# Kernel tuning notes

Hardware: AMD Instinct MI355X
Metric: run time of the kernel (lower is better)

The kernel has to match this reference:

```python
import jax, jax.numpy as jnp
import numpy as np

NU, NI, NA = 100000, 50000, 5000
FEAT, H, L = 256, 128, 2
E_RATES, E_SIM, E_HAS = 1000000, 500000, 250000
SCALE = 0.05


def setup_inputs() -> dict:
    key = jax.random.key(0)
    ks = jax.random.split(key, 20)
    f32 = jnp.float32
    inp = {}
    inp["x_item_feat"] = jax.random.normal(ks[0], (NI, FEAT), f32)
    inp["user_emb"] = jax.random.normal(ks[1], (NU, H), f32) * SCALE
    inp["attr_emb"] = jax.random.normal(ks[2], (NA, H), f32) * SCALE
    inp["lin_item_W"] = jax.random.normal(ks[3], (FEAT, H), f32) * SCALE
    inp["lin_item_b"] = jnp.zeros((H,), f32)
    inp["ui_Wl"] = jax.random.normal(ks[4], (L, 4, H, H), f32) * SCALE
    inp["ui_bl"] = jnp.zeros((L, 4, H), f32)
    inp["ui_Wr"] = jax.random.normal(ks[5], (L, 4, H, H), f32) * SCALE
    inp["ii_Wl"] = jax.random.normal(ks[6], (L, 2, H, H), f32) * SCALE
    inp["ii_bl"] = jnp.zeros((L, 2, H), f32)
    inp["ii_Wr"] = jax.random.normal(ks[7], (L, 2, H, H), f32) * SCALE
    inp["ia_Wl"] = jax.random.normal(ks[8], (L, 4, H, H), f32) * SCALE
    inp["ia_bl"] = jnp.zeros((L, 4, H), f32)
    inp["ia_Wr"] = jax.random.normal(ks[9], (L, 4, H, H), f32) * SCALE
    inp["alpha"] = jnp.zeros((3,), f32)
    # edge_index rows: [src; dst], ranges per node type
    inp["edge_rates"] = jnp.stack([
        jax.random.randint(ks[10], (E_RATES,), 0, NU, jnp.int32),   # user src
        jax.random.randint(ks[11], (E_RATES,), 0, NI, jnp.int32)])  # item dst
    inp["edge_sim"] = jnp.stack([
        jax.random.randint(ks[12], (E_SIM,), 0, NI, jnp.int32),
        jax.random.randint(ks[13], (E_SIM,), 0, NI, jnp.int32)])
    inp["edge_has"] = jnp.stack([
        jax.random.randint(ks[14], (E_HAS,), 0, NI, jnp.int32),    # item src
        jax.random.randint(ks[15], (E_HAS,), 0, NA, jnp.int32)])   # attr dst
    return inp


def _sage_edge(x_src, x_dst, src, dst, Wl, bl, Wr):
    # PyG SAGEConv: lin_l(mean of neighbor messages) + lin_r(root)
    n_dst = x_dst.shape[0]
    agg = jax.ops.segment_sum(x_src[src], dst, num_segments=n_dst)
    cnt = jax.ops.segment_sum(jnp.ones(src.shape[0], x_src.dtype), dst, num_segments=n_dst)
    agg = agg / jnp.maximum(cnt, 1.0)[:, None]
    return agg @ Wl + bl + x_dst @ Wr


def _sage_self(x, Wl, bl, Wr):
    # 'self' relation realized as identity self-loops: mean aggr of single self neighbor = x
    return x @ Wl + bl + x @ Wr


def reference(x_item_feat, user_emb, attr_emb, lin_item_W, lin_item_b,
              ui_Wl, ui_bl, ui_Wr, ii_Wl, ii_bl, ii_Wr, ia_Wl, ia_bl, ia_Wr,
              alpha, edge_rates, edge_sim, edge_has):
    x_item = x_item_feat @ lin_item_W + lin_item_b
    relu = jax.nn.relu

    # user-item branch (relations: 0=rates u->i, 1=rev_rates i->u, 2=user self, 3=item self)
    hu, hi = user_emb, x_item
    for l in range(L):
        o_i = 0.5 * (_sage_edge(hu, hi, edge_rates[0], edge_rates[1], ui_Wl[l, 0], ui_bl[l, 0], ui_Wr[l, 0])
                     + _sage_self(hi, ui_Wl[l, 3], ui_bl[l, 3], ui_Wr[l, 3]))
        o_u = 0.5 * (_sage_edge(hi, hu, edge_rates[1], edge_rates[0], ui_Wl[l, 1], ui_bl[l, 1], ui_Wr[l, 1])
                     + _sage_self(hu, ui_Wl[l, 2], ui_bl[l, 2], ui_Wr[l, 2]))
        hu, hi = relu(o_u), relu(o_i)
    h_ui_item = hi

    # item-item content branch (0=sim, 1=item self)
    h = x_item
    for l in range(L):
        o = 0.5 * (_sage_edge(h, h, edge_sim[0], edge_sim[1], ii_Wl[l, 0], ii_bl[l, 0], ii_Wr[l, 0])
                   + _sage_self(h, ii_Wl[l, 1], ii_bl[l, 1], ii_Wr[l, 1]))
        h = relu(o)
    h_ii_item = h

    # item-attr branch (0=has i->a, 1=rev_has a->i, 2=item self, 3=attr self)
    hi2, ha = x_item, attr_emb
    for l in range(L):
        o_a = 0.5 * (_sage_edge(hi2, ha, edge_has[0], edge_has[1], ia_Wl[l, 0], ia_bl[l, 0], ia_Wr[l, 0])
                     + _sage_self(ha, ia_Wl[l, 3], ia_bl[l, 3], ia_Wr[l, 3]))
        o_i = 0.5 * (_sage_edge(ha, hi2, edge_has[1], edge_has[0], ia_Wl[l, 1], ia_bl[l, 1], ia_Wr[l, 1])
                     + _sage_self(hi2, ia_Wl[l, 2], ia_bl[l, 2], ia_Wr[l, 2]))
        hi2, ha = relu(o_i), relu(o_a)
    h_ia_item = hi2

    w = jax.nn.softmax(alpha)
    h_fused = w[0] * h_ui_item + w[1] * h_ii_item + w[2] * h_ia_item
    return (h_fused, h_ui_item, h_ii_item, h_ia_item, w)
```

## Files before the change

kernel.cpp:

```cpp
#include <hip/hip_runtime.h>

#define NU_ 100000
#define NI_ 50000
#define NA_ 5000
#define FEAT_ 256
#define H_ 128
#define ER_ 1000000
#define ES_ 500000
#define EH_ 250000

#define NTOT_ (3 * NI_ + NU_ + NA_)
#define RTOT_ (2 * ER_ + ES_ + 2 * EH_)
#define NSB_ ((NTOT_ + 1023) / 1024)
#define B_RI 0
#define B_RU (NI_)
#define B_SI (NI_ + NU_)
#define B_HA (2 * NI_ + NU_)
#define B_HI (2 * NI_ + NU_ + NA_)

typedef long long i64;
typedef unsigned short u16;
typedef unsigned int u32;
typedef __attribute__((ext_vector_type(8))) short bf16x8;
typedef __attribute__((ext_vector_type(4))) float f32x4;

__device__ __forceinline__ u16 f2bf(float v) {
    u32 b = __float_as_uint(v);
    b += 0x7fff + ((b >> 16) & 1);
    return (u16)(b >> 16);
}
__device__ __forceinline__ float bf2f(u16 v) {
    return __uint_as_float((u32)v << 16);
}

__global__ __launch_bounds__(256) void tobf2_kernel(const float4* __restrict__ inU,
                                                    ushort4* __restrict__ outU, long n4u,
                                                    const float4* __restrict__ inA,
                                                    ushort4* __restrict__ outA, long n4a) {
    long i = (long)blockIdx.x * 256 + threadIdx.x;
    const float4* in; ushort4* out;
    if (i < n4u) { in = inU + i; out = outU + i; }
    else if (i < n4u + n4a) { in = inA + (i - n4u); out = outA + (i - n4u); }
    else return;
    float4 v = *in;
    ushort4 o;
    o.x = f2bf(v.x); o.y = f2bf(v.y); o.z = f2bf(v.z); o.w = f2bf(v.w);
    *out = o;
}

__device__ __forceinline__ void rec_of(int r, const int* __restrict__ er,
                                       const int* __restrict__ es,
                                       const int* __restrict__ eh,
                                       int& node, int& val) {
    if (r < 2 * ER_) {
        int e = r >> 1;
        if ((r & 1) == 0) { node = B_RI + er[ER_ + e]; val = er[e]; }
        else              { node = B_RU + er[e];       val = er[ER_ + e]; }
    } else if (r < 2 * ER_ + ES_) {
        int e = r - 2 * ER_;
        node = B_SI + es[ES_ + e]; val = es[e];
    } else {
        int q = r - 2 * ER_ - ES_;
        int e = q >> 1;
        if ((q & 1) == 0) { node = B_HA + eh[EH_ + e]; val = eh[e]; }
        else              { node = B_HI + eh[e];       val = eh[EH_ + e]; }
    }
}

__global__ __launch_bounds__(256) void sbinit_kernel(int* __restrict__ sbc,
                                                     int* __restrict__ OFF) {
    int t = threadIdx.x;
    sbc[t] = t << 16;
    if (t < 4) OFF[t] = 0;
}

__global__ __launch_bounds__(256) void binA_kernel(const int* __restrict__ er,
                                                   const int* __restrict__ es,
                                                   const int* __restrict__ eh,
                                                   int* __restrict__ sbc,
                                                   int* __restrict__ cpool) {
    __shared__ int h[256];
    __shared__ int gof[256];
    int t = threadIdx.x;
    h[t] = 0;
    __syncthreads();
    int base = blockIdx.x * 4096;
    int sbs[16];
    u32 recs[16];
#pragma unroll
    for (int i = 0; i < 16; ++i) {
        int r = base + i * 256 + t;
        sbs[i] = -1;
        if (r < RTOT_) {
            int node, val;
            rec_of(r, er, es, eh, node, val);
            int sb = node >> 10;
            sbs[i] = sb;
            recs[i] = ((u32)(node & 1023) << 17) | (u32)val;
            atomicAdd(&h[sb], 1);
        }
    }
    __syncthreads();
    {
        int c = h[t];
        if (c > 0) gof[t] = atomicAdd(&sbc[t], c);
        h[t] = 0;
    }
    __syncthreads();
#pragma unroll
    for (int i = 0; i < 16; ++i) {
        if (sbs[i] >= 0) {
            int slot = atomicAdd(&h[sbs[i]], 1);
            cpool[gof[sbs[i]] + slot] = (int)recs[i];
        }
    }
}

__global__ __launch_bounds__(256) void sbscan_kernel(const int* __restrict__ sbc,
                                                     int* __restrict__ sbb) {
    int t = threadIdx.x;
    int v = (t < NSB_) ? (sbc[t] - (t << 16)) : 0;
    int incl = v;
    int lane = t & 63;
#pragma unroll
    for (int d = 1; d < 64; d <<= 1) {
        int u = __shfl_up(incl, d);
        if (lane >= d) incl += u;
    }
    __shared__ int wsum[4];
    if (lane == 63) wsum[t >> 6] = incl;
    __syncthreads();
    int wo = 0;
    for (int i = 0; i < (t >> 6); ++i) wo += wsum[i];
    if (t < NSB_) sbb[t] = wo + incl - v;
}

__global__ __launch_bounds__(1024) void binB_kernel(const int* __restrict__ cpool,
                                                    const int* __restrict__ sbb,
                                                    const int* __restrict__ sbc,
                                                    int* __restrict__ off1,
                                                    int* __restrict__ pool) {
    __shared__ int c[1024];
    __shared__ int b[1024];
    __shared__ int wsum[16];
    int sb = blockIdx.x, t = threadIdx.x;
    int rlo = sb << 16, rhi = sbc[sb];
    int base = sbb[sb];
    c[t] = 0;
    __syncthreads();
    for (int j = rlo + t; j < rhi; j += 1024)
        atomicAdd(&c[((u32)cpool[j]) >> 17], 1);
    __syncthreads();
    int v = c[t];
    int incl = v;
    int lane = t & 63;
#pragma unroll
    for (int d = 1; d < 64; d <<= 1) {
        int u = __shfl_up(incl, d);
        if (lane >= d) incl += u;
    }
    if (lane == 63) wsum[t >> 6] = incl;
    __syncthreads();
    int wo = 0;
    for (int i = 0; i < (t >> 6); ++i) wo += wsum[i];
    int ex = wo + incl - v;
    int node = sb * 1024 + t;
    if (node < NTOT_) off1[node] = base + ex + v;
    b[t] = base + ex;
    __syncthreads();
    for (int j = rlo + t; j < rhi; j += 1024) {
        u32 rec = (u32)cpool[j];
        int pos = atomicAdd(&b[rec >> 17], 1);
        pool[pos] = (int)(rec & 0x1FFFF);
    }
}

struct WJob {
    const float* s0; const float* s1; const float* s2;
    int logK; int base;
};
struct WJobs { WJob j[17]; };

__global__ __launch_bounds__(256) void wsplit_kernel(WJobs jobs, int njobs, int total,
                                                     u16* __restrict__ WTH,
                                                     u16* __restrict__ WTL) {
    int gid = blockIdx.x * 256 + threadIdx.x;
    if (gid >= total) return;
    int ji = 0;
    for (int i = 1; i < 17; ++i)
        if (i < njobs && gid >= jobs.j[i].base) ji = i;
    WJob jb = jobs.j[ji];
    int local = gid - jb.base;
    int e = local & 7;
    int l = (local >> 3) & 63;
    int nt = (local >> 9) & 7;
    int kc = local >> 12;
    int n = nt * 16 + (l & 15);
    int k = kc * 32 + ((l >> 4) << 3) + e;
    i64 si = (i64)k * 128 + n;
    float v = jb.s0[si];
    if (jb.s1 != nullptr) v += jb.s1[si] + jb.s2[si];
    if (jb.logK == 8) {
        u32 b = __float_as_uint(v);
        u16 h = (u16)(b >> 16);
        float rem = v - __uint_as_float(b & 0xffff0000u);
        WTH[gid] = h;
        WTL[gid] = (u16)(__float_as_uint(rem) >> 16);
    } else {
        WTH[gid] = f2bf(v);
    }
}

#define ACC8(A, V)                                                            \
    {                                                                         \
        A[0] += bf2f((u16)(V.x & 0xffff)); A[1] += bf2f((u16)(V.x >> 16));    \
        A[2] += bf2f((u16)(V.y & 0xffff)); A[3] += bf2f((u16)(V.y >> 16));    \
        A[4] += bf2f((u16)(V.z & 0xffff)); A[5] += bf2f((u16)(V.z >> 16));    \
        A[6] += bf2f((u16)(V.w & 0xffff)); A[7] += bf2f((u16)(V.w >> 16));    \
    }

struct GOp {
    const u16* feat; const int* off1c; u16* agg;
    int nblk; int n; int pad0; int pad1; int pad2;
};
struct GOps { GOp op[5]; };

__global__ __launch_bounds__(256) void packed_gather_kernel(GOps ops, int nops,
                                                            const int* __restrict__ pool) {
    int b = blockIdx.x;
    int i = 0;
    while (i < nops - 1 && b >= ops.op[i].nblk) { b -= ops.op[i].nblk; ++i; }
    GOp o = ops.op[i];
    int row = b * 16 + (threadIdx.x >> 4);
    if (row >= o.n) return;
    int lane = (threadIdx.x & 15) * 8;
    int start = o.off1c[row - 1];
    int end = o.off1c[row];
    const u16* feat = o.feat;
    float a0[8], a1[8], a2[8], a3[8];
#pragma unroll
    for (int k = 0; k < 8; ++k) { a0[k] = 0.f; a1[k] = 0.f; a2[k] = 0.f; a3[k] = 0.f; }
    int j = start;
    for (; j + 4 <= end; j += 4) {
        int s0 = pool[j], s1 = pool[j + 1], s2 = pool[j + 2], s3 = pool[j + 3];
        uint4 v0 = *(const uint4*)&feat[(i64)s0 * H_ + lane];
        uint4 v1 = *(const uint4*)&feat[(i64)s1 * H_ + lane];
        uint4 v2 = *(const uint4*)&feat[(i64)s2 * H_ + lane];
        uint4 v3 = *(const uint4*)&feat[(i64)s3 * H_ + lane];
        ACC8(a0, v0); ACC8(a1, v1); ACC8(a2, v2); ACC8(a3, v3);
    }
    for (; j < end; ++j) {
        int s0 = pool[j];
        uint4 v0 = *(const uint4*)&feat[(i64)s0 * H_ + lane];
        ACC8(a0, v0);
    }
    float inv = 1.0f / fmaxf((float)(end - start), 1.0f);
    uint4 o4;
    float r0, r1;
    r0 = (a0[0] + a1[0] + a2[0] + a3[0]) * inv; r1 = (a0[1] + a1[1] + a2[1] + a3[1]) * inv;
    o4.x = (u32)f2bf(r0) | ((u32)f2bf(r1) << 16);
    r0 = (a0[2] + a1[2] + a2[2] + a3[2]) * inv; r1 = (a0[3] + a1[3] + a2[3] + a3[3]) * inv;
    o4.y = (u32)f2bf(r0) | ((u32)f2bf(r1) << 16);
    r0 = (a0[4] + a1[4] + a2[4] + a3[4]) * inv; r1 = (a0[5] + a1[5] + a2[5] + a3[5]) * inv;
    o4.z = (u32)f2bf(r0) | ((u32)f2bf(r1) << 16);
    r0 = (a0[6] + a1[6] + a2[6] + a3[6]) * inv; r1 = (a0[7] + a1[7] + a2[7] + a3[7]) * inv;
    o4.w = (u32)f2bf(r0) | ((u32)f2bf(r1) << 16);
    *(uint4*)&o.agg[(i64)row * H_ + lane] = o4;
}

__device__ __forceinline__ void split8(const float* f, bf16x8& h, bf16x8& lo) {
#pragma unroll
    for (int i = 0; i < 8; ++i) {
        u32 b = __float_as_uint(f[i]);
        h[i] = (short)(u16)(b >> 16);
        float rem = f[i] - __uint_as_float(b & 0xffff0000u);
        lo[i] = (short)(u16)(__float_as_uint(rem) >> 16);
    }
}

__global__ __launch_bounds__(256) void mgemm_x_kernel(
    const float* __restrict__ A, const u16* __restrict__ Wh, const u16* __restrict__ Wl,
    const float* __restrict__ bias, u16* __restrict__ Cbf, int M) {
    int t = threadIdx.x;
    int w = t >> 6, l = t & 63;
    int lr = l & 15, lq = l >> 4;
    int m0 = blockIdx.x * 128 + w * 32;

    f32x4 acc[2][8];
#pragma unroll
    for (int mt = 0; mt < 2; ++mt)
#pragma unroll
        for (int nt = 0; nt < 8; ++nt) acc[mt][nt] = (f32x4){0.f, 0.f, 0.f, 0.f};

    for (int kc = 0; kc < 8; ++kc) {
        bf16x8 ah0, al0, ah1, al1;
        {
            int row = m0 + lr;
            float f[8];
            if (row < M) {
                const float* ap = &A[(i64)row * FEAT_ + kc * 32 + lq * 8];
                *(float4*)&f[0] = *(const float4*)ap;
                *(float4*)&f[4] = *(const float4*)(ap + 4);
            } else {
#pragma unroll
                for (int i = 0; i < 8; ++i) f[i] = 0.f;
            }
            split8(f, ah0, al0);
        }
        {
            int row = m0 + 16 + lr;
            float f[8];
            if (row < M) {
                const float* ap = &A[(i64)row * FEAT_ + kc * 32 + lq * 8];
                *(float4*)&f[0] = *(const float4*)ap;
                *(float4*)&f[4] = *(const float4*)(ap + 4);
            } else {
#pragma unroll
                for (int i = 0; i < 8; ++i) f[i] = 0.f;
            }
            split8(f, ah1, al1);
        }
        const u16* whp = Wh + ((i64)kc * 8) * 512 + (i64)l * 8;
        const u16* wlp = Wl + ((i64)kc * 8) * 512 + (i64)l * 8;
#pragma unroll
        for (int nt = 0; nt < 8; ++nt) {
            bf16x8 bh = *(const bf16x8*)(whp + nt * 512);
            bf16x8 bl = *(const bf16x8*)(wlp + nt * 512);
            acc[0][nt] = __builtin_amdgcn_mfma_f32_16x16x32_bf16(ah0, bh, acc[0][nt], 0, 0, 0);
            acc[1][nt] = __builtin_amdgcn_mfma_f32_16x16x32_bf16(ah1, bh, acc[1][nt], 0, 0, 0);
            acc[0][nt] = __builtin_amdgcn_mfma_f32_16x16x32_bf16(al0, bh, acc[0][nt], 0, 0, 0);
            acc[1][nt] = __builtin_amdgcn_mfma_f32_16x16x32_bf16(al1, bh, acc[1][nt], 0, 0, 0);
            acc[0][nt] = __builtin_amdgcn_mfma_f32_16x16x32_bf16(ah0, bl, acc[0][nt], 0, 0, 0);
            acc[1][nt] = __builtin_amdgcn_mfma_f32_16x16x32_bf16(ah1, bl, acc[1][nt], 0, 0, 0);
        }
    }
#pragma unroll
    for (int nt = 0; nt < 8; ++nt) {
        int col = nt * 16 + lr;
        float bb = bias[col];
#pragma unroll
        for (int mt = 0; mt < 2; ++mt) {
#pragma unroll
            for (int r = 0; r < 4; ++r) {
                int row = m0 + mt * 16 + (lq << 2) + r;
                if (row < M) Cbf[(i64)row * H_ + col] = f2bf(acc[mt][nt][r] + bb);
            }
        }
    }
}

struct MOp {
    const u16* A1; const u16* W1; const u16* A2; const u16* W2;
    const float* b1; const float* b2;
    float* C; u16* Cbf;
    int nblk; int n; int fuse; int pad;
};
struct MOps { MOp op[5]; };

__global__ __launch_bounds__(256) void packed_gemm_kernel(
    MOps ops, int nops,
    const float* __restrict__ alpha, const float* __restrict__ fu,
    const float* __restrict__ fi, float* __restrict__ fout,
    float* __restrict__ wout) {
    int blk = blockIdx.x;
    int i = 0;
    while (i < nops - 1 && blk >= ops.op[i].nblk) { blk -= ops.op[i].nblk; ++i; }
    MOp o = ops.op[i];
    int t = threadIdx.x;
    int w = t >> 6, l = t & 63;
    int lr = l & 15, lq = l >> 4;
    int m0 = blk * 128 + w * 32;
    int M = o.n;

    f32x4 acc[2][8];
#pragma unroll
    for (int mt = 0; mt < 2; ++mt)
#pragma unroll
        for (int nt = 0; nt < 8; ++nt) acc[mt][nt] = (f32x4){0.f, 0.f, 0.f, 0.f};

#pragma unroll
    for (int mat = 0; mat < 2; ++mat) {
        const u16* A = mat ? o.A2 : o.A1;
        const u16* W = mat ? o.W2 : o.W1;
#pragma unroll
        for (int kc = 0; kc < 4; ++kc) {
            bf16x8 a0 = {0, 0, 0, 0, 0, 0, 0, 0}, a1 = {0, 0, 0, 0, 0, 0, 0, 0};
            int row0 = m0 + lr, row1 = m0 + 16 + lr;
            if (row0 < M) a0 = *(const bf16x8*)&A[(i64)row0 * H_ + kc * 32 + lq * 8];
            if (row1 < M) a1 = *(const bf16x8*)&A[(i64)row1 * H_ + kc * 32 + lq * 8];
            const u16* wp = W + ((i64)kc * 8) * 512 + (i64)l * 8;
#pragma unroll
            for (int nt = 0; nt < 8; ++nt) {
                bf16x8 bw = *(const bf16x8*)(wp + nt * 512);
                acc[0][nt] = __builtin_amdgcn_mfma_f32_16x16x32_bf16(a0, bw, acc[0][nt], 0, 0, 0);
                acc[1][nt] = __builtin_amdgcn_mfma_f32_16x16x32_bf16(a1, bw, acc[1][nt], 0, 0, 0);
            }
        }
    }

    float w0 = 0.f, w1 = 0.f, w2 = 0.f;
    if (o.fuse) {
        float x0 = alpha[0], x1 = alpha[1], x2 = alpha[2];
        float mx = fmaxf(x0, fmaxf(x1, x2));
        float e0 = __expf(x0 - mx), e1 = __expf(x1 - mx), e2 = __expf(x2 - mx);
        float inv = 1.f / (e0 + e1 + e2);
        w0 = e0 * inv; w1 = e1 * inv; w2 = e2 * inv;
        if (blk == 0 && t == 0) { wout[0] = w0; wout[1] = w1; wout[2] = w2; }
    }

#pragma unroll
    for (int nt = 0; nt < 8; ++nt) {
        int col = nt * 16 + lr;
        float bb = 0.5f * (o.b1[col] + o.b2[col]);
#pragma unroll
        for (int mt = 0; mt < 2; ++mt) {
#pragma unroll
            for (int r = 0; r < 4; ++r) {
                int row = m0 + mt * 16 + (lq << 2) + r;
                if (row < M) {
                    i64 idx = (i64)row * H_ + col;
                    float v = fmaxf(0.5f * acc[mt][nt][r] + bb, 0.f);
                    if (o.C != nullptr) o.C[idx] = v;
                    if (o.Cbf != nullptr) o.Cbf[idx] = f2bf(v);
                    if (o.fuse) fout[idx] = w0 * fu[idx] + w1 * fi[idx] + w2 * v;
                }
            }
        }
    }
}

extern "C" void kernel_launch(void* const* d_in, const int* in_sizes, int n_in,
                              void* d_out, int out_size, void* d_ws, size_t ws_size,
                              hipStream_t stream) {
    const float* xif  = (const float*)d_in[0];
    const float* uemb = (const float*)d_in[1];
    const float* aemb = (const float*)d_in[2];
    const float* liW  = (const float*)d_in[3];
    const float* lib  = (const float*)d_in[4];
    const float* uiWl = (const float*)d_in[5];
    const float* uibl = (const float*)d_in[6];
    const float* uiWr = (const float*)d_in[7];
    const float* iiWl = (const float*)d_in[8];
    const float* iibl = (const float*)d_in[9];
    const float* iiWr = (const float*)d_in[10];
    const float* iaWl = (const float*)d_in[11];
    const float* iabl = (const float*)d_in[12];
    const float* iaWr = (const float*)d_in[13];
    const float* alpha = (const float*)d_in[14];
    const int* er = (const int*)d_in[15];
    const int* es = (const int*)d_in[16];
    const int* eh = (const int*)d_in[17];

    float* out = (float*)d_out;
    float* FUSED  = out;
    float* OUT_UI = out + (i64)NI_ * H_;
    float* OUT_II = out + (i64)2 * NI_ * H_;
    float* OUT_IA = out + (i64)3 * NI_ * H_;
    float* WOUT   = out + (i64)4 * NI_ * H_;

    u16* u = (u16*)d_ws;
    i64 uo = 0;
    u16* WTH    = u + uo; uo += 294912;
    u16* WTL    = u + uo; uo += 294912;
    u16* X_bf   = u + uo; uo += (i64)NI_ * H_;
    u16* HIU_bf = u + uo; uo += (i64)NI_ * H_;
    u16* HII_bf = u + uo; uo += (i64)NI_ * H_;
    u16* HIA_bf = u + uo; uo += (i64)NI_ * H_;
    u16* HU1_bf = u + uo; uo += (i64)NU_ * H_;
    u16* HA1_bf = u + uo; uo += (i64)NA_ * H_;
    u16* UE_bf  = u + uo; uo += (i64)NU_ * H_;
    u16* AE_bf  = u + uo; uo += (i64)NA_ * H_;
    u16* AGG1 = u + uo; uo += (i64)NI_ * H_;
    u16* AGG2 = u + uo; uo += (i64)NU_ * H_;
    u16* AGG3 = u + uo; uo += (i64)NI_ * H_;
    u16* AGG4 = u + uo; uo += (i64)NI_ * H_;
    u16* AGG5 = u + uo; uo += (i64)NI_ * H_;
    u16* AGG6 = u + uo; uo += (i64)NA_ * H_;
    u16* AGG7 = u + uo; uo += (i64)NI_ * H_;
    u16* AGG8 = u + uo; uo += (i64)NI_ * H_;

    int* ip = (int*)(u + uo);
    i64 io = 0;
    int* OFF   = ip + io; io += NTOT_ + 4;
    int* SBB   = ip + io; io += 256;
    int* SBC   = ip + io; io += 256;
    int* POOL  = ip + io; io += RTOT_;
    int* CPOOL = ip + io; io += (i64)NSB_ << 16;
    int* off1 = OFF + 1;

    {
        sbinit_kernel<<<1, 256, 0, stream>>>(SBC, OFF);
        int nblk = (RTOT_ + 4095) / 4096;
        binA_kernel<<<nblk, 256, 0, stream>>>(er, es, eh, SBC, CPOOL);
        sbscan_kernel<<<1, 256, 0, stream>>>(SBC, SBB);
        binB_kernel<<<NSB_, 1024, 0, stream>>>(CPOOL, SBB, SBC, off1, POOL);
    }

    const float* famWl[8] = {uiWl, uiWl, uiWl, iiWl, iiWl, iaWl, iaWl, iaWl};
    const float* famWr[8] = {uiWr, uiWr, uiWr, iiWr, iiWr, iaWr, iaWr, iaWr};
    const float* famBl[8] = {uibl, uibl, uibl, iibl, iibl, iabl, iabl, iabl};
    const int eidx[8] = {0, 1, 4, 0, 2, 0, 1, 5};
    const int sidx[8] = {3, 2, 7, 1, 3, 3, 2, 6};

    WJobs jobs;
    jobs.j[0] = {liW, nullptr, nullptr, 8, 0};
    int base = 32768;
    for (int s = 0; s < 8; ++s) {
        jobs.j[1 + 2 * s] = {famWl[s] + (i64)eidx[s] * 16384, nullptr, nullptr, 7, base};
        base += 16384;
        jobs.j[2 + 2 * s] = {famWr[s] + (i64)eidx[s] * 16384,
                             famWl[s] + (i64)sidx[s] * 16384,
                             famWr[s] + (i64)sidx[s] * 16384, 7, base};
        base += 16384;
    }
    wsplit_kernel<<<(base + 255) / 256, 256, 0, stream>>>(jobs, 17, base, WTH, WTL);

    long n4u = (long)NU_ * H_ / 4, n4a = (long)NA_ * H_ / 4;
    tobf2_kernel<<<(int)((n4u + n4a + 255) / 256), 256, 0, stream>>>(
        (const float4*)uemb, (ushort4*)UE_bf, n4u,
        (const float4*)aemb, (ushort4*)AE_bf, n4a);

    mgemm_x_kernel<<<(NI_ + 127) / 128, 256, 0, stream>>>(xif, WTH, WTL, lib, X_bf, NI_);

    auto mkg = [&](const u16* feat, int cbase, int n, u16* agg) {
        GOp o{};
        o.feat = feat; o.off1c = off1 + cbase; o.agg = agg;
        o.nblk = (n + 15) / 16; o.n = n;
        return o;
    };
    auto glaunch = [&](GOps& ops, int nops) {
        int grid = 0;
        for (int i = 0; i < nops; ++i) grid += ops.op[i].nblk;
        packed_gather_kernel<<<grid, 256, 0, stream>>>(ops, nops, POOL);
    };
    auto mkm = [&](int slot, const u16* agg, const u16* A2, float* C, u16* Cbf,
                   int M, int fuse) {
        MOp o{};
        o.A1 = agg;
        o.W1 = WTH + 32768 + (i64)(2 * slot) * 16384;
        o.A2 = A2;
        o.W2 = WTH + 32768 + (i64)(2 * slot + 1) * 16384;
        o.b1 = famBl[slot] + (i64)eidx[slot] * 128;
        o.b2 = famBl[slot] + (i64)sidx[slot] * 128;
        o.C = C; o.Cbf = Cbf;
        o.nblk = (M + 127) / 128; o.n = M; o.fuse = fuse;
        return o;
    };
    auto mlaunch = [&](MOps& ops, int nops) {
        int grid = 0;
        for (int i = 0; i < nops; ++i) grid += ops.op[i].nblk;
        packed_gemm_kernel<<<grid, 256, 0, stream>>>(ops, nops, alpha,
                                                     OUT_UI, OUT_II, FUSED, WOUT);
    };

    {
        GOps g{};
        g.op[0] = mkg(X_bf, B_HA, NA_, AGG6);
        g.op[1] = mkg(UE_bf, B_RI, NI_, AGG1);
        g.op[2] = mkg(X_bf, B_RU, NU_, AGG2);
        g.op[3] = mkg(X_bf, B_SI, NI_, AGG4);
        g.op[4] = mkg(AE_bf, B_HI, NI_, AGG7);
        glaunch(g, 5);
    }
    {
        MOps m{};
        m.op[0] = mkm(1, AGG2, UE_bf, nullptr, HU1_bf, NU_, 0);
        m.op[1] = mkm(0, AGG1, X_bf, nullptr, HIU_bf, NI_, 0);
        m.op[2] = mkm(3, AGG4, X_bf, nullptr, HII_bf, NI_, 0);
        m.op[3] = mkm(6, AGG7, X_bf, nullptr, HIA_bf, NI_, 0);
        m.op[4] = mkm(5, AGG6, AE_bf, nullptr, HA1_bf, NA_, 0);
        mlaunch(m, 5);
    }
    {
        GOps g{};
        g.op[0] = mkg(HU1_bf, B_RI, NI_, AGG3);
        g.op[1] = mkg(HII_bf, B_SI, NI_, AGG5);
        g.op[2] = mkg(HA1_bf, B_HI, NI_, AGG8);
        glaunch(g, 3);
    }
    {
        MOps m{};
        m.op[0] = mkm(2, AGG3, HIU_bf, OUT_UI, nullptr, NI_, 0);
        m.op[1] = mkm(4, AGG5, HII_bf, OUT_II, nullptr, NI_, 0);
        mlaunch(m, 2);
    }
    {
        MOps m{};
        m.op[0] = mkm(7, AGG8, HIA_bf, OUT_IA, nullptr, NI_, 1);
        mlaunch(m, 1);
    }
}
```

Measured before the change: 498.1 us.

## Merge setup kernels into one launch and split gather edges across wavefront

Folds the edge-binning pass, the fp32-to-bf16 embedding conversion and the weight split/repack into a single block-partitioned kernel, removing two launches and letting these independent jobs run concurrently. The neighbor gather now assigns a whole 64-lane wavefront to each destination row, with four edge groups processed in parallel and combined by cross-lane shuffles, instead of 16 threads per row walking edges serially. This shortens the per-row dependency chain for high-degree rows and spreads the work over more waves. In exchange, low-degree rows leave lanes idle and each row pays extra shuffle reductions.

Measured after the change: 527.1 us. 5.8% more time.

```diff
diff --git a/kernel.cpp b/kernel.cpp
--- a/kernel.cpp
+++ b/kernel.cpp
@@ -31,21 +31,6 @@
 }
 __device__ __forceinline__ float bf2f(u16 v) {
     return __uint_as_float((u32)v << 16);
-}
-
-__global__ __launch_bounds__(256) void tobf2_kernel(const float4* __restrict__ inU,
-                                                    ushort4* __restrict__ outU, long n4u,
-                                                    const float4* __restrict__ inA,
-                                                    ushort4* __restrict__ outA, long n4a) {
-    long i = (long)blockIdx.x * 256 + threadIdx.x;
-    const float4* in; ushort4* out;
-    if (i < n4u) { in = inU + i; out = outU + i; }
-    else if (i < n4u + n4a) { in = inA + (i - n4u); out = outA + (i - n4u); }
-    else return;
-    float4 v = *in;
-    ushort4 o;
-    o.x = f2bf(v.x); o.y = f2bf(v.y); o.z = f2bf(v.z); o.w = f2bf(v.w);
-    *out = o;
 }
 
 __device__ __forceinline__ void rec_of(int r, const int* __restrict__ er,
@@ -74,44 +59,96 @@
     if (t < 4) OFF[t] = 0;
 }
 
-__global__ __launch_bounds__(256) void binA_kernel(const int* __restrict__ er,
-                                                   const int* __restrict__ es,
-                                                   const int* __restrict__ eh,
-                                                   int* __restrict__ sbc,
-                                                   int* __restrict__ cpool) {
+struct WJob {
+    const float* s0; const float* s1; const float* s2;
+    int logK; int base;
+};
+struct WJobs { WJob j[17]; };
+
+__global__ __launch_bounds__(256) void packed_misc_kernel(
+    const int* __restrict__ er, const int* __restrict__ es, const int* __restrict__ eh,
+    int* __restrict__ sbc, int* __restrict__ cpool, int nblkA,
+    const float4* __restrict__ inU, ushort4* __restrict__ outU, long n4u,
+    const float4* __restrict__ inA, ushort4* __restrict__ outA, long n4a, int nblkT,
+    WJobs jobs, int wtotal, u16* __restrict__ WTH, u16* __restrict__ WTL) {
     __shared__ int h[256];
     __shared__ int gof[256];
+    int b = blockIdx.x;
     int t = threadIdx.x;
-    h[t] = 0;
-    __syncthreads();
-    int base = blockIdx.x * 4096;
-    int sbs[16];
-    u32 recs[16];
-#pragma unroll
-    for (int i = 0; i < 16; ++i) {
-        int r = base + i * 256 + t;
-        sbs[i] = -1;
-        if (r < RTOT_) {
-            int node, val;
-            rec_of(r, er, es, eh, node, val);
-            int sb = node >> 10;
-            sbs[i] = sb;
-            recs[i] = ((u32)(node & 1023) << 17) | (u32)val;
-            atomicAdd(&h[sb], 1);
-        }
-    }
-    __syncthreads();
+    if (b < nblkA) {
+        h[t] = 0;
+        __syncthreads();
+        int base = b * 4096;
+        int sbs[16];
+        u32 recs[16];
+#pragma unroll
+        for (int i = 0; i < 16; ++i) {
+            int r = base + i * 256 + t;
+            sbs[i] = -1;
+            if (r < RTOT_) {
+                int node, val;
+                rec_of(r, er, es, eh, node, val);
+                int sb = node >> 10;
+                sbs[i] = sb;
+                recs[i] = ((u32)(node & 1023) << 17) | (u32)val;
+                atomicAdd(&h[sb], 1);
+            }
+        }
+        __syncthreads();
+        {
+            int c = h[t];
+            if (c > 0) gof[t] = atomicAdd(&sbc[t], c);
+            h[t] = 0;
+        }
+        __syncthreads();
+#pragma unroll
+        for (int i = 0; i < 16; ++i) {
+            if (sbs[i] >= 0) {
+                int slot = atomicAdd(&h[sbs[i]], 1);
+                cpool[gof[sbs[i]] + slot] = (int)recs[i];
+            }
+        }
+        return;
+    }
+    b -= nblkA;
+    if (b < nblkT) {
+        long i = (long)b * 256 + t;
+        const float4* in; ushort4* out;
+        if (i < n4u) { in = inU + i; out = outU + i; }
+        else if (i < n4u + n4a) { in = inA + (i - n4u); out = outA + (i - n4u); }
+        else return;
+        float4 v = *in;
+        ushort4 o;
+        o.x = f2bf(v.x); o.y = f2bf(v.y); o.z = f2bf(v.z); o.w = f2bf(v.w);
+        *out = o;
+        return;
+    }
+    b -= nblkT;
     {
-        int c = h[t];
-        if (c > 0) gof[t] = atomicAdd(&sbc[t], c);
-        h[t] = 0;
-    }
-    __syncthreads();
-#pragma unroll
-    for (int i = 0; i < 16; ++i) {
-        if (sbs[i] >= 0) {
-            int slot = atomicAdd(&h[sbs[i]], 1);
-            cpool[gof[sbs[i]] + slot] = (int)recs[i];
+        int gid = b * 256 + t;
+        if (gid >= wtotal) return;
+        int ji = 0;
+        for (int i = 1; i < 17; ++i)
+            if (gid >= jobs.j[i].base) ji = i;
+        WJob jb = jobs.j[ji];
+        int local = gid - jb.base;
+        int e = local & 7;
+        int l = (local >> 3) & 63;
+        int nt = (local >> 9) & 7;
+        int kc = local >> 12;
+        int n = nt * 16 + (l & 15);
+        int k = kc * 32 + ((l >> 4) << 3) + e;
+        i64 si = (i64)k * 128 + n;
+        float v = jb.s0[si];
+        if (jb.s1 != nullptr) v += jb.s1[si] + jb.s2[si];
+        if (jb.logK == 8) {
+            u32 bb = __float_as_uint(v);
+            u16 hh = (u16)(bb >> 16);
+            float rem = v - __uint_as_float(bb & 0xffff0000u);
+            WTH[gid] = hh;
+            WTL[gid] = (u16)(__float_as_uint(rem) >> 16);
+        } else {
+            WTH[gid] = f2bf(v);
         }
     }
 }
@@ -175,42 +212,6 @@
     }
 }
 
-struct WJob {
-    const float* s0; const float* s1; const float* s2;
-    int logK; int base;
-};
-struct WJobs { WJob j[17]; };
-
-__global__ __launch_bounds__(256) void wsplit_kernel(WJobs jobs, int njobs, int total,
-                                                     u16* __restrict__ WTH,
-                                                     u16* __restrict__ WTL) {
-    int gid = blockIdx.x * 256 + threadIdx.x;
-    if (gid >= total) return;
-    int ji = 0;
-    for (int i = 1; i < 17; ++i)
-        if (i < njobs && gid >= jobs.j[i].base) ji = i;
-    WJob jb = jobs.j[ji];
-    int local = gid - jb.base;
-    int e = local & 7;
-    int l = (local >> 3) & 63;
-    int nt = (local >> 9) & 7;
-    int kc = local >> 12;
-    int n = nt * 16 + (l & 15);
-    int k = kc * 32 + ((l >> 4) << 3) + e;
-    i64 si = (i64)k * 128 + n;
-    float v = jb.s0[si];
-    if (jb.s1 != nullptr) v += jb.s1[si] + jb.s2[si];
-    if (jb.logK == 8) {
-        u32 b = __float_as_uint(v);
-        u16 h = (u16)(b >> 16);
-        float rem = v - __uint_as_float(b & 0xffff0000u);
-        WTH[gid] = h;
-        WTL[gid] = (u16)(__float_as_uint(rem) >> 16);
-    } else {
-        WTH[gid] = f2bf(v);
-    }
-}
-
 #define ACC8(A, V)                                                            \
     {                                                                         \
         A[0] += bf2f((u16)(V.x & 0xffff)); A[1] += bf2f((u16)(V.x >> 16));    \
@@ -231,41 +232,47 @@
     int i = 0;
     while (i < nops - 1 && b >= ops.op[i].nblk) { b -= ops.op[i].nblk; ++i; }
     GOp o = ops.op[i];
-    int row = b * 16 + (threadIdx.x >> 4);
+    int t = threadIdx.x;
+    int row = b * 4 + (t >> 6);
     if (row >= o.n) return;
-    int lane = (threadIdx.x & 15) * 8;
+    int l = t & 63;
+    int eg = l >> 4;
+    int lane = (l & 15) * 8;
     int start = o.off1c[row - 1];
     int end = o.off1c[row];
     const u16* feat = o.feat;
-    float a0[8], a1[8], a2[8], a3[8];
-#pragma unroll
-    for (int k = 0; k < 8; ++k) { a0[k] = 0.f; a1[k] = 0.f; a2[k] = 0.f; a3[k] = 0.f; }
-    int j = start;
-    for (; j + 4 <= end; j += 4) {
-        int s0 = pool[j], s1 = pool[j + 1], s2 = pool[j + 2], s3 = pool[j + 3];
-        uint4 v0 = *(const uint4*)&feat[(i64)s0 * H_ + lane];
-        uint4 v1 = *(const uint4*)&feat[(i64)s1 * H_ + lane];
-        uint4 v2 = *(const uint4*)&feat[(i64)s2 * H_ + lane];
-        uint4 v3 = *(const uint4*)&feat[(i64)s3 * H_ + lane];
-        ACC8(a0, v0); ACC8(a1, v1); ACC8(a2, v2); ACC8(a3, v3);
-    }
-    for (; j < end; ++j) {
-        int s0 = pool[j];
-        uint4 v0 = *(const uint4*)&feat[(i64)s0 * H_ + lane];
-        ACC8(a0, v0);
-    }
-    float inv = 1.0f / fmaxf((float)(end - start), 1.0f);
-    uint4 o4;
-    float r0, r1;
-    r0 = (a0[0] + a1[0] + a2[0] + a3[0]) * inv; r1 = (a0[1] + a1[1] + a2[1] + a3[1]) * inv;
-    o4.x = (u32)f2bf(r0) | ((u32)f2bf(r1) << 16);
-    r0 = (a0[2] + a1[2] + a2[2] + a3[2]) * inv; r1 = (a0[3] + a1[3] + a2[3] + a3[3]) * inv;
-    o4.y = (u32)f2bf(r0) | ((u32)f2bf(r1) << 16);
-    r0 = (a0[4] + a1[4] + a2[4] + a3[4]) * inv; r1 = (a0[5] + a1[5] + a2[5] + a3[5]) * inv;
-    o4.z = (u32)f2bf(r0) | ((u32)f2bf(r1) << 16);
-    r0 = (a0[6] + a1[6] + a2[6] + a3[6]) * inv; r1 = (a0[7] + a1[7] + a2[7] + a3[7]) * inv;
-    o4.w = (u32)f2bf(r0) | ((u32)f2bf(r1) << 16);
-    *(uint4*)&o.agg[(i64)row * H_ + lane] = o4;
+    float a0[8], a1[8];
+#pragma unroll
+    for (int k = 0; k < 8; ++k) { a0[k] = 0.f; a1[k] = 0.f; }
+    for (int j0 = start; j0 < end; j0 += 8) {
+        int ja = j0 + eg, jb = j0 + 4 + eg;
+        if (ja < end) {
+            int s = pool[ja];
+            uint4 v = *(const uint4*)&feat[(i64)s * H_ + lane];
+            ACC8(a0, v);
+        }
+        if (jb < end) {
+            int s = pool[jb];
+            uint4 v = *(const uint4*)&feat[(i64)s * H_ + lane];
+            ACC8(a1, v);
+        }
+    }
+#pragma unroll
+    for (int k = 0; k < 8; ++k) {
+        float s = a0[k] + a1[k];
+        s += __shfl_xor(s, 16);
+        s += __shfl_xor(s, 32);
+        a0[k] = s;
+    }
+    if (eg == 0) {
+        float inv = 1.0f / fmaxf((float)(end - start), 1.0f);
+        uint4 o4;
+        o4.x = (u32)f2bf(a0[0] * inv) | ((u32)f2bf(a0[1] * inv) << 16);
+        o4.y = (u32)f2bf(a0[2] * inv) | ((u32)f2bf(a0[3] * inv) << 16);
+        o4.z = (u32)f2bf(a0[4] * inv) | ((u32)f2bf(a0[5] * inv) << 16);
+        o4.w = (u32)f2bf(a0[6] * inv) | ((u32)f2bf(a0[7] * inv) << 16);
+        *(uint4*)&o.agg[(i64)row * H_ + lane] = o4;
+    }
 }
 
 __device__ __forceinline__ void split8(const float* f, bf16x8& h, bf16x8& lo) {
@@ -488,14 +495,6 @@
     int* CPOOL = ip + io; io += (i64)NSB_ << 16;
     int* off1 = OFF + 1;
 
-    {
-        sbinit_kernel<<<1, 256, 0, stream>>>(SBC, OFF);
-        int nblk = (RTOT_ + 4095) / 4096;
-        binA_kernel<<<nblk, 256, 0, stream>>>(er, es, eh, SBC, CPOOL);
-        sbscan_kernel<<<1, 256, 0, stream>>>(SBC, SBB);
-        binB_kernel<<<NSB_, 1024, 0, stream>>>(CPOOL, SBB, SBC, off1, POOL);
-    }
-
     const float* famWl[8] = {uiWl, uiWl, uiWl, iiWl, iiWl, iaWl, iaWl, iaWl};
     const float* famWr[8] = {uiWr, uiWr, uiWr, iiWr, iiWr, iaWr, iaWr, iaWr};
     const float* famBl[8] = {uibl, uibl, uibl, iibl, iibl, iabl, iabl, iabl};
@@ -504,28 +503,35 @@
 
     WJobs jobs;
     jobs.j[0] = {liW, nullptr, nullptr, 8, 0};
-    int base = 32768;
+    int wtotal = 32768;
     for (int s = 0; s < 8; ++s) {
-        jobs.j[1 + 2 * s] = {famWl[s] + (i64)eidx[s] * 16384, nullptr, nullptr, 7, base};
-        base += 16384;
+        jobs.j[1 + 2 * s] = {famWl[s] + (i64)eidx[s] * 16384, nullptr, nullptr, 7, wtotal};
+        wtotal += 16384;
         jobs.j[2 + 2 * s] = {famWr[s] + (i64)eidx[s] * 16384,
                              famWl[s] + (i64)sidx[s] * 16384,
-                             famWr[s] + (i64)sidx[s] * 16384, 7, base};
-        base += 16384;
-    }
-    wsplit_kernel<<<(base + 255) / 256, 256, 0, stream>>>(jobs, 17, base, WTH, WTL);
-
+                             famWr[s] + (i64)sidx[s] * 16384, 7, wtotal};
+        wtotal += 16384;
+    }
+
+    sbinit_kernel<<<1, 256, 0, stream>>>(SBC, OFF);
     long n4u = (long)NU_ * H_ / 4, n4a = (long)NA_ * H_ / 4;
-    tobf2_kernel<<<(int)((n4u + n4a + 255) / 256), 256, 0, stream>>>(
+    int nblkA = (RTOT_ + 4095) / 4096;
+    int nblkT = (int)((n4u + n4a + 255) / 256);
+    int nblkW = (wtotal + 255) / 256;
+    packed_misc_kernel<<<nblkA + nblkT + nblkW, 256, 0, stream>>>(
+        er, es, eh, SBC, CPOOL, nblkA,
         (const float4*)uemb, (ushort4*)UE_bf, n4u,
-        (const float4*)aemb, (ushort4*)AE_bf, n4a);
+        (const float4*)aemb, (ushort4*)AE_bf, n4a, nblkT,
+        jobs, wtotal, WTH, WTL);
+    sbscan_kernel<<<1, 256, 0, stream>>>(SBC, SBB);
+    binB_kernel<<<NSB_, 1024, 0, stream>>>(CPOOL, SBB, SBC, off1, POOL);
 
     mgemm_x_kernel<<<(NI_ + 127) / 128, 256, 0, stream>>>(xif, WTH, WTL, lib, X_bf, NI_);
 
     auto mkg = [&](const u16* feat, int cbase, int n, u16* agg) {
         GOp o{};
         o.feat = feat; o.off1c = off1 + cbase; o.agg = agg;
-        o.nblk = (n + 15) / 16; o.n = n;
+        o.nblk = (n + 3) / 4; o.n = n;
         return o;
     };
     auto glaunch = [&](GOps& ops, int nops) {
```
